# Kernel tuning notes

Hardware: AMD Instinct MI355X
Metric: run time of the kernel (lower is better)

The kernel has to match this reference:

```python
import jax, jax.numpy as jnp
import numpy as np

B, I, O = 1024, 512, 512
EPS = 1e-07
LOG_CLIP = 20.0

def setup_inputs() -> dict:
    key = jax.random.key(0)
    k1, k2, k3, k4 = jax.random.split(key, 4)
    x = jax.random.normal(k1, (B, I), dtype=jnp.float32)
    # match tf.random_normal_initializer(mean, stddev) used in the layer
    w_hat = 0.88 + 0.2 * jax.random.normal(k2, (I, O), dtype=jnp.float32)
    m_hat = 0.5 + 0.2 * jax.random.normal(k3, (I, O), dtype=jnp.float32)
    g = 0.2 * jax.random.normal(k4, (O,), dtype=jnp.float32)
    return {"x": x, "w_hat": w_hat, "m_hat": m_hat, "g": g}

def reference(x, w_hat, m_hat, g):
    w1 = jnp.tanh(w_hat) * jax.nn.sigmoid(m_hat)          # [I, O]
    a = x @ w1                                             # [B, O] additive path
    # multiplicative path: exp(log|x| @ w1), clipped at 20 before exp
    logx = jnp.log(jnp.maximum(jnp.abs(x), EPS))           # [B, I]
    m1 = jnp.exp(jnp.minimum(logx @ w1, LOG_CLIP))         # [B, O]
    # sign-product tracking. TF flattens w1 row-major to [I*O], tiles x
    # O times along axis 1 -> xs[b, k] = x[b, k % I]; so after reshape to
    # [B, O, I], the paired weight magnitude is ws[j, i] = |w1.flat[j*I + i]|.
    ws_oi = jnp.abs(w1.reshape(-1)).reshape(O, I)          # [O, I] (faithful to TF reshape)
    sgn_x = jnp.sign(x)                                    # [B, I]
    sgn = sgn_x[:, None, :] * ws_oi[None, :, :] + (1.0 - ws_oi)[None, :, :]  # [B, O, I]
    ms = jnp.prod(sgn, axis=2)                             # [B, O]
    g1 = jax.nn.sigmoid(g)                                 # [O]
    return g1 * a + (1.0 - g1) * m1 * jnp.clip(ms, -1.0, 1.0)
```

## Files before the change

kernel.cpp:

```cpp
#include <hip/hip_runtime.h>


#define O_N 512
#define I_N 512
#define B_N 1024

typedef _Float16 f16;
typedef _Float16 f16x8 __attribute__((ext_vector_type(8)));
typedef float f32x4 __attribute__((ext_vector_type(4)));

__device__ __forceinline__ float fast_sigmoid(float v) {
    return 1.0f / (1.0f + __expf(-v));
}
__device__ __forceinline__ float fast_tanh(float v) {
    return 1.0f - 2.0f / (1.0f + __expf(2.0f * v));
}

__global__ __launch_bounds__(256) void prep_kernel(const float* __restrict__ x,
                                                   const float* __restrict__ wh,
                                                   const float* __restrict__ mh,
                                                   f16x8* __restrict__ apx,
                                                   f16x8* __restrict__ apl,
                                                   f16x8* __restrict__ bp) {
    const int tid = threadIdx.x;
    if (blockIdx.x < 128) {
        __shared__ f16 lt[32][72];
        const int kb = blockIdx.x >> 3;
        const int nb = blockIdx.x & 7;
        const int r  = tid >> 3;
        const int c0 = (tid & 7) * 8;
        const int base = (kb * 32 + r) * O_N + nb * 64 + c0;
        const float4* w4 = (const float4*)(wh + base);
        const float4* m4 = (const float4*)(mh + base);
        const float4 wa = w4[0], wb = w4[1], ma = m4[0], mb = m4[1];
        f16x8 row;
        row[0] = (f16)(fast_tanh(wa.x) * fast_sigmoid(ma.x));
        row[1] = (f16)(fast_tanh(wa.y) * fast_sigmoid(ma.y));
        row[2] = (f16)(fast_tanh(wa.z) * fast_sigmoid(ma.z));
        row[3] = (f16)(fast_tanh(wa.w) * fast_sigmoid(ma.w));
        row[4] = (f16)(fast_tanh(wb.x) * fast_sigmoid(mb.x));
        row[5] = (f16)(fast_tanh(wb.y) * fast_sigmoid(mb.y));
        row[6] = (f16)(fast_tanh(wb.z) * fast_sigmoid(mb.z));
        row[7] = (f16)(fast_tanh(wb.w) * fast_sigmoid(mb.w));
        *(f16x8*)&lt[r][c0] = row;
        __syncthreads();
        const int fl  = tid & 63;
        const int tnl = tid >> 6;
        const int nl  = tnl * 16 + (fl & 15);
        const int k0  = (fl >> 4) * 8;
        f16x8 bf;
#pragma unroll
        for (int j = 0; j < 8; ++j) bf[j] = lt[k0 + j][nl];
        const int tn_g = nb * 4 + tnl;
        bp[tn_g * 1024 + kb * 64 + fl] = bf;
    } else {
        const int t  = (blockIdx.x - 128) * 256 + tid;
        const int fl = t & 63;
        const int tk = (t >> 6) & 15;
        const int tm = t >> 10;
        const int m  = tm * 16 + (fl & 15);
        const int k0 = tk * 32 + (fl >> 4) * 8;
        const float4* x4 = (const float4*)(x + m * I_N + k0);
        const float4 q0 = x4[0], q1 = x4[1];
        const float vx[8] = {q0.x, q0.y, q0.z, q0.w, q1.x, q1.y, q1.z, q1.w};
        f16x8 fx, fv;
#pragma unroll
        for (int j = 0; j < 8; ++j) {
            fx[j] = (f16)vx[j];
            fv[j] = (f16)__logf(fmaxf(fabsf(vx[j]), 1e-7f));
        }
        apx[t] = fx;
        apl[t] = fv;
    }
}

__global__ __launch_bounds__(256) void nalu_mfma_kernel(const f16x8* __restrict__ apx,
                                                        const f16x8* __restrict__ apl,
                                                        const f16x8* __restrict__ bp,
                                                        const float* __restrict__ g,
                                                        const float* __restrict__ x,
                                                        const float* __restrict__ wh,
                                                        const float* __restrict__ mh,
                                                        float* __restrict__ out) {
    const int lane = threadIdx.x & 63;
    const int w    = threadIdx.x >> 6;
    const int b0   = blockIdx.y * 32 + (w & 1) * 16;
    const int o0   = blockIdx.x * 32 + (w >> 1) * 16;
    const int tm   = b0 >> 4;
    const int tn   = o0 >> 4;

    f32x4 ca = {0.f, 0.f, 0.f, 0.f}, cs = ca;

    const f16x8* pax = apx + tm * 1024 + lane;
    const f16x8* pal = apl + tm * 1024 + lane;
    const f16x8* pbp = bp  + tn * 1024 + lane;

#pragma unroll 8
    for (int tk = 0; tk < 16; ++tk) {
        const f16x8 ax = pax[tk * 64];
        const f16x8 al = pal[tk * 64];
        const f16x8 bf = pbp[tk * 64];
        ca = __builtin_amdgcn_mfma_f32_16x16x32_f16(ax, bf, ca, 0, 0, 0);
        cs = __builtin_amdgcn_mfma_f32_16x16x32_f16(al, bf, cs, 0, 0, 0);
    }

    const int col = lane & 15;
    const int rq  = (lane >> 4) * 4;
    const int o   = o0 + col;
    const float g1  = fast_sigmoid(g[o]);
    const float omg = 1.0f - g1;
#pragma unroll
    for (int r = 0; r < 4; ++r) {
        const int b = b0 + rq + r;
        const float sv = cs[r];
        const float m1 = __expf(fminf(sv, 20.0f));
        float msv = 1.0f;
        if (sv > -80.0f) {
            float p = 1.0f;
            for (int i = 0; i < I_N; ++i) {
                const float wv = fabsf(fast_tanh(wh[o * I_N + i]) *
                                       fast_sigmoid(mh[o * I_N + i]));
                const float xv = x[b * I_N + i];
                const float sg = (xv > 0.f) ? 1.f : ((xv < 0.f) ? -1.f : 0.f);
                p *= sg * wv + (1.0f - wv);
            }
            msv = fminf(fmaxf(p, -1.0f), 1.0f);
        }
        out[b * O_N + o] = g1 * ca[r] + omg * m1 * msv;
    }
}

extern "C" void kernel_launch(void* const* d_in, const int* in_sizes, int n_in,
                              void* d_out, int out_size, void* d_ws, size_t ws_size,
                              hipStream_t stream) {
    const float* x  = (const float*)d_in[0];
    const float* wh = (const float*)d_in[1];
    const float* mh = (const float*)d_in[2];
    const float* g  = (const float*)d_in[3];
    float* out = (float*)d_out;

    char* ws = (char*)d_ws;
    f16x8* apx = (f16x8*)ws;
    f16x8* apl = (f16x8*)(ws + (1u << 20));
    f16x8* bp  = (f16x8*)(ws + (2u << 20));

    prep_kernel<<<384, 256, 0, stream>>>(x, wh, mh, apx, apl, bp);
    nalu_mfma_kernel<<<dim3(16, 32), 256, 0, stream>>>(apx, apl, bp, g, x, wh, mh, out);
}
```

Before: 68.82 us.

## Split additive and log GEMMs across separate waves, exchange via LDS

Each wave now computes a single MFMA accumulation, either the additive x@w1 or the log-path log|x|@w1, instead of both. The grid doubles to 16-row batch tiles, and the log-path results pass through shared memory to the additive waves, which run the epilogue. The aim is more waves in flight and a shorter dependent MFMA chain per wave, at the cost of a __syncthreads, LDS traffic and half the waves sitting idle during the epilogue. Launch bounds also now request 4 blocks per CU.

```diff
diff --git a/kernel.cpp b/kernel.cpp
--- a/kernel.cpp
+++ b/kernel.cpp
@@ -74,59 +74,69 @@
     }
 }
 
-__global__ __launch_bounds__(256) void nalu_mfma_kernel(const f16x8* __restrict__ apx,
-                                                        const f16x8* __restrict__ apl,
-                                                        const f16x8* __restrict__ bp,
-                                                        const float* __restrict__ g,
-                                                        const float* __restrict__ x,
-                                                        const float* __restrict__ wh,
-                                                        const float* __restrict__ mh,
-                                                        float* __restrict__ out) {
+__global__ __launch_bounds__(256, 4) void nalu_mfma_kernel(const f16x8* __restrict__ apx,
+                                                           const f16x8* __restrict__ apl,
+                                                           const f16x8* __restrict__ bp,
+                                                           const float* __restrict__ g,
+                                                           const float* __restrict__ x,
+                                                           const float* __restrict__ wh,
+                                                           const float* __restrict__ mh,
+                                                           float* __restrict__ out) {
+    __shared__ float scs[2][16][17];
+
     const int lane = threadIdx.x & 63;
     const int w    = threadIdx.x >> 6;
-    const int b0   = blockIdx.y * 32 + (w & 1) * 16;
-    const int o0   = blockIdx.x * 32 + (w >> 1) * 16;
-    const int tm   = b0 >> 4;
+    const int isS  = w & 1;
+    const int osub = w >> 1;
+    const int b0   = blockIdx.y * 16;
+    const int o0   = blockIdx.x * 32 + osub * 16;
+    const int tm   = blockIdx.y;
     const int tn   = o0 >> 4;
 
-    f32x4 ca = {0.f, 0.f, 0.f, 0.f}, cs = ca;
+    f32x4 acc = {0.f, 0.f, 0.f, 0.f};
 
-    const f16x8* pax = apx + tm * 1024 + lane;
-    const f16x8* pal = apl + tm * 1024 + lane;
-    const f16x8* pbp = bp  + tn * 1024 + lane;
+    const f16x8* pa = (isS ? apl : apx) + tm * 1024 + lane;
+    const f16x8* pb = bp + tn * 1024 + lane;
 
 #pragma unroll 8
     for (int tk = 0; tk < 16; ++tk) {
-        const f16x8 ax = pax[tk * 64];
-        const f16x8 al = pal[tk * 64];
-        const f16x8 bf = pbp[tk * 64];
-        ca = __builtin_amdgcn_mfma_f32_16x16x32_f16(ax, bf, ca, 0, 0, 0);
-        cs = __builtin_amdgcn_mfma_f32_16x16x32_f16(al, bf, cs, 0, 0, 0);
+        const f16x8 av = pa[tk * 64];
+        const f16x8 bv = pb[tk * 64];
+        acc = __builtin_amdgcn_mfma_f32_16x16x32_f16(av, bv, acc, 0, 0, 0);
     }
 
     const int col = lane & 15;
     const int rq  = (lane >> 4) * 4;
-    const int o   = o0 + col;
-    const float g1  = fast_sigmoid(g[o]);
-    const float omg = 1.0f - g1;
+
+    if (isS) {
 #pragma unroll
-    for (int r = 0; r < 4; ++r) {
-        const int b = b0 + rq + r;
-        const float sv = cs[r];
-        const float m1 = __expf(fminf(sv, 20.0f));
-        float msv = 1.0f;
-        if (sv > -80.0f) {
-            float p = 1.0f;
-            for (int i = 0; i < I_N; ++i) {
-                const float wv = fabsf(fast_tanh(wh[o * I_N + i]) *
-                                       fast_sigmoid(mh[o * I_N + i]));
-                const float xv = x[b * I_N + i];
-                const float sg = (xv > 0.f) ? 1.f : ((xv < 0.f) ? -1.f : 0.f);
-                p *= sg * wv + (1.0f - wv);
+        for (int r = 0; r < 4; ++r) scs[osub][rq + r][col] = acc[r];
+    }
+    __syncthreads();
+
+    if (!isS) {
+        const int o = o0 + col;
+        const float g1  = fast_sigmoid(g[o]);
+        const float omg = 1.0f - g1;
+#pragma unroll
+        for (int r = 0; r < 4; ++r) {
+            const int b = b0 + rq + r;
+            const float sv = scs[osub][rq + r][col];
+            const float m1 = __expf(fminf(sv, 20.0f));
+            float msv = 1.0f;
+            if (sv > -80.0f) {
+                float p = 1.0f;
+                for (int i = 0; i < I_N; ++i) {
+                    const float wv = fabsf(fast_tanh(wh[o * I_N + i]) *
+                                           fast_sigmoid(mh[o * I_N + i]));
+                    const float xv = x[b * I_N + i];
+                    const float sg = (xv > 0.f) ? 1.f : ((xv < 0.f) ? -1.f : 0.f);
+                    p *= sg * wv + (1.0f - wv);
+                }
+                msv = fminf(fmaxf(p, -1.0f), 1.0f);
             }
-            msv = fminf(fmaxf(p, -1.0f), 1.0f);
+            out[b * O_N + o] = g1 * acc[r] + omg * m1 * msv;
         }
-        out[b * O_N + o] = g1 * ca[r] + omg * m1 * msv;
     }
 }
 
@@ -145,5 +155,5 @@
     f16x8* bp  = (f16x8*)(ws + (2u << 20));
 
     prep_kernel<<<384, 256, 0, stream>>>(x, wh, mh, apx, apl, bp);
-    nalu_mfma_kernel<<<dim3(16, 32), 256, 0, stream>>>(apx, apl, bp, g, x, wh, mh, out);
+    nalu_mfma_kernel<<<dim3(16, 64), 256, 0, stream>>>(apx, apl, bp, g, x, wh, mh, out);
 }
```

New measurement: 69.27 us. Within noise of the previous version (+0.6%).
